# Performance work log

Measured on AMD Instinct MI355X. Metric: run time of the kernel, lower is better.

The kernel has to match this reference:

```python
import jax, jax.numpy as jnp
import numpy as np

NUM_NODES = 64
NUM_VISIBLE = 16
NUM_STEPS = 20
ENERGY_SCALE = 1.0


def setup_inputs() -> dict:
    key = jax.random.key(0)
    k1, k2, k3, k4 = jax.random.split(key, 4)
    B, E = 65536, 512
    embedding = jax.random.normal(k1, (B, E), dtype=jnp.float32)
    reward = jax.random.normal(k2, (B,), dtype=jnp.float32)
    pca_components = jax.random.normal(k3, (E, NUM_VISIBLE), dtype=jnp.float32)
    quadratic = jax.random.normal(k4, (NUM_NODES, NUM_NODES), dtype=jnp.float32) * 0.01
    return {"embedding": embedding, "reward": reward,
            "pca_components": pca_components, "quadratic": quadratic}


def reference(embedding, reward, pca_components, quadratic):
    B = embedding.shape[0]
    dtype = embedding.dtype

    # KPP fallback transform: PCA-style projection (B, E) @ (E, 16) -> (B, 16)
    rep = embedding @ pca_components
    visible_bias = rep[:, :NUM_VISIBLE]

    # per-sample linear bias, zeros except visible slots; BM bias = batch mean (no_grad)
    lb = jnp.zeros((B, NUM_NODES), dtype).at[:, :NUM_VISIBLE].set(visible_bias)
    b = jax.lax.stop_gradient(lb.mean(axis=0))  # (N,)

    # clamped visible state: sigmoid(2*r) broadcast to (B, NUM_VISIBLE)
    s_visible = jnp.broadcast_to(jax.nn.sigmoid(reward[:, None] * 2.0), (B, NUM_VISIBLE))

    Wsym = quadratic + quadratic.T  # symmetric coupling field

    key = jax.random.key(42)
    k_init, k_scan = jax.random.split(key)
    hidden0 = jax.random.bernoulli(k_init, 0.5, (B, NUM_NODES - NUM_VISIBLE)).astype(dtype)
    s0 = jnp.concatenate([s_visible, hidden0], axis=-1)  # (B, N)

    def gibbs_step(s, k):
        p = jax.nn.sigmoid(s @ Wsym + b)               # (B, N)
        s_new = jax.random.bernoulli(k, p).astype(dtype)
        s_new = s_new.at[:, :NUM_VISIBLE].set(s_visible)  # clamp visible units
        return s_new, None

    keys = jax.random.split(k_scan, NUM_STEPS)
    s_all, _ = jax.lax.scan(gibbs_step, s0, keys)

    # energy E(s) = -s^T Q s - b^T s  per sample
    energy = -jnp.einsum('bi,ij,bj->b', s_all, quadratic, s_all) - s_all @ b

    adjusted = reward - ENERGY_SCALE * energy
    return adjusted[:, None]  # (B, 1)
```

## Files before the change

### kernel.cpp

```cpp
#include <hip/hip_runtime.h>
#include <stdint.h>

#define NNODES 64
#define NVIS   16
#define NHID   48
#define NSTEPS 20
#define BATCH  65536
#define EDIM   512

typedef float f32x2 __attribute__((ext_vector_type(2)));
typedef float f32x4 __attribute__((ext_vector_type(4)));

__device__ __forceinline__ f32x2 pk_fma_lo(f32x2 s, f32x2 w, f32x2 c) {
  f32x2 d;
  asm("v_pk_fma_f32 %0, %1, %2, %3 op_sel:[0,0,0] op_sel_hi:[1,0,1]"
      : "=v"(d) : "v"(s), "v"(w), "v"(c));
  return d;
}
__device__ __forceinline__ f32x2 pk_fma_hi(f32x2 s, f32x2 w, f32x2 c) {
  f32x2 d;
  asm("v_pk_fma_f32 %0, %1, %2, %3 op_sel:[0,1,0] op_sel_hi:[1,1,1]"
      : "=v"(d) : "v"(s), "v"(w), "v"(c));
  return d;
}
__device__ __forceinline__ f32x2 pk_fma2(f32x2 a, f32x2 b, f32x2 c) {
  f32x2 d;
  asm("v_pk_fma_f32 %0, %1, %2, %3" : "=v"(d) : "v"(a), "v"(b), "v"(c));
  return d;
}
__device__ __forceinline__ f32x2 pk_mul2(f32x2 a, f32x2 b) {
  f32x2 d;
  asm("v_pk_mul_f32 %0, %1, %2" : "=v"(d) : "v"(a), "v"(b));
  return d;
}
__device__ __forceinline__ f32x2 pk_add2(f32x2 a, f32x2 b) {
  f32x2 d;
  asm("v_pk_add_f32 %0, %1, %2" : "=v"(d) : "v"(a), "v"(b));
  return d;
}
__device__ __forceinline__ f32x2 pk_sub2(f32x2 a, f32x2 b) {
  f32x2 d;
  asm("v_pk_add_f32 %0, %1, %2 neg_lo:[0,1] neg_hi:[0,1]" : "=v"(d) : "v"(a), "v"(b));
  return d;
}
__device__ __forceinline__ f32x2 pk_negsub2(f32x2 a, f32x2 b) {
  f32x2 d;
  asm("v_pk_add_f32 %0, %1, %2 neg_lo:[1,1] neg_hi:[1,1]" : "=v"(d) : "v"(a), "v"(b));
  return d;
}

__device__ __forceinline__ void tf2x32(uint32_t k0, uint32_t k1,
                                       uint32_t x0, uint32_t x1,
                                       uint32_t& o0, uint32_t& o1) {
  const uint32_t ks0 = k0, ks1 = k1, ks2 = k0 ^ k1 ^ 0x1BD11BDAu;
  x0 += ks0; x1 += ks1;
  const int rotA[4] = {13, 15, 26, 6};
  const int rotB[4] = {17, 29, 16, 24};
#pragma unroll
  for (int i = 0; i < 5; ++i) {
#pragma unroll
    for (int r = 0; r < 4; ++r) {
      const int rot = (i & 1) ? rotB[r] : rotA[r];
      x0 += x1;
      x1 = __builtin_rotateleft32(x1, rot);
      x1 ^= x0;
    }
    const uint32_t i0 = (i == 0 || i == 3) ? ks1 : (i == 1 || i == 4) ? ks2 : ks0;
    const uint32_t i1 = (i == 0 || i == 3) ? ks2 : (i == 1 || i == 4) ? ks0 : ks1;
    x0 += i0;
    x1 += i1 + (uint32_t)(i + 1);
  }
  o0 = x0; o1 = x1;
}

__device__ __forceinline__ uint32_t rbits32(uint32_t k0, uint32_t k1, uint32_t n) {
  uint32_t a, b;
  tf2x32(k0, k1, 0u, n, a, b);
  return a ^ b;
}

__device__ __forceinline__ f32x2 sigmoid2_pk(f32x2 a) {
#pragma clang fp contract(off)
  const f32x2 cL2En  = (f32x2)(-1.44269504088896341f);
  const f32x2 cHalf  = (f32x2)0.5f;
  const f32x2 cLn2Hi = (f32x2)0.693359375f;
  const f32x2 cLn2Lo = (f32x2)(-2.12194440e-4f);
  const f32x2 c0 = (f32x2)1.9875691500e-4f, c1 = (f32x2)1.3981999507e-3f;
  const f32x2 c2 = (f32x2)8.3334519073e-3f, c3 = (f32x2)4.1665795894e-2f;
  const f32x2 c4 = (f32x2)1.6666665459e-1f, c5 = (f32x2)5.0000001201e-1f;
  const f32x2 cOne = (f32x2)1.0f;

  f32x2 t = pk_fma2(a, cL2En, cHalf);
  f32x2 fx; fx.x = floorf(t.x); fx.y = floorf(t.y);
  f32x2 tmp = pk_mul2(fx, cLn2Hi);
  f32x2 z   = pk_mul2(fx, cLn2Lo);
  f32x2 xr  = pk_negsub2(a, tmp);
  xr = pk_sub2(xr, z);
  f32x2 zz = pk_mul2(xr, xr);
  f32x2 y = pk_fma2(xr, c0, c1);
  y = pk_fma2(y, xr, c2);
  y = pk_fma2(y, xr, c3);
  y = pk_fma2(y, xr, c4);
  y = pk_fma2(y, xr, c5);
  y = pk_fma2(y, zz, xr);
  y = pk_add2(y, cOne);
  int mx = (int)fx.x, my = (int)fx.y;
  f32x2 e;
  e.x = __int_as_float((mx + 127) << 23);
  e.y = __int_as_float((my + 127) << 23);
  f32x2 ex = pk_mul2(y, e);
  f32x2 den = pk_add2(ex, cOne);
  f32x2 r;
  r.x = 1.0f / den.x;
  r.y = 1.0f / den.y;
  return r;
}

__device__ __forceinline__ f32x2 dot_hidden(const f32x4* __restrict__ swq,
                                            const f32x2* wp, f32x2 acc16) {
  f32x2 acc = acc16;
#pragma unroll
  for (int i = 0; i < 24; ++i) {
    f32x4 q = swq[i];
    f32x2 slo; slo.x = q.x; slo.y = q.y;
    f32x2 shi; shi.x = q.z; shi.y = q.w;
    acc = pk_fma_lo(slo, wp[i], acc);
    acc = pk_fma_hi(shi, wp[i], acc);
  }
  return acc;
}

__global__ __launch_bounds__(512) void colsum_kernel(const float4* __restrict__ emb4,
                                                     float4* __restrict__ partials4,
                                                     int nblk) {
  __shared__ float4 red[4][128];
  const int t = threadIdx.x;
  const int c4 = t & 127, rs = t >> 7;
  float4 acc = make_float4(0.f, 0.f, 0.f, 0.f);
  const int stride = nblk * 4;
  for (int r = blockIdx.x * 4 + rs; r < BATCH; r += stride) {
    float4 v = emb4[(size_t)r * 128 + c4];
    acc.x += v.x; acc.y += v.y; acc.z += v.z; acc.w += v.w;
  }
  red[rs][c4] = acc;
  __syncthreads();
  if (rs == 0) {
    float4 a = red[0][c4], b = red[1][c4], c = red[2][c4], d = red[3][c4];
    float4 s;
    s.x = (a.x + b.x) + (c.x + d.x);
    s.y = (a.y + b.y) + (c.y + d.y);
    s.z = (a.z + b.z) + (c.z + d.z);
    s.w = (a.w + b.w) + (c.w + d.w);
    partials4[(size_t)blockIdx.x * 128 + c4] = s;
  }
}

__global__ __launch_bounds__(512) void reduce_kernel(const float* __restrict__ partials,
                                                     float* __restrict__ level2, int per) {
  const int t = threadIdx.x;
  float a = 0.0f;
  const int s0 = blockIdx.x * per;
  for (int s = s0; s < s0 + per; ++s) a += partials[(size_t)s * EDIM + t];
  level2[(size_t)blockIdx.x * EDIM + t] = a;
}

__global__ __launch_bounds__(512) void prep_kernel(const float* __restrict__ pca,
                                                   const float* __restrict__ level2, int g2,
                                                   float* __restrict__ bvec,
                                                   unsigned* __restrict__ keys) {
  __shared__ float cs[EDIM];
  int t = threadIdx.x;
  float a = 0.0f;
  for (int i = 0; i < g2; ++i) a += level2[(size_t)i * EDIM + t];
  cs[t] = a;
  __syncthreads();
  if (t < NNODES) {
    float bj = 0.0f;
    if (t < NVIS) {
      for (int e = 0; e < EDIM; ++e) bj = fmaf(cs[e], pca[e * NVIS + t], bj);
      bj *= (1.0f / 65536.0f);
    }
    bvec[t] = bj;
  }
  if (t == 0) {
    uint32_t ki0, ki1, ks0, ks1;
    tf2x32(0u, 42u, 0u, 0u, ki0, ki1);
    tf2x32(0u, 42u, 0u, 1u, ks0, ks1);
    keys[0] = ki0; keys[1] = ki1;
    for (int s = 0; s < NSTEPS; ++s) {
      uint32_t y0, y1;
      tf2x32(ks0, ks1, 0u, (uint32_t)s, y0, y1);
      keys[2 + 2 * s] = y0;
      keys[3 + 2 * s] = y1;
    }
  }
}

__global__ __launch_bounds__(256) void gibbs_kernel(const float* __restrict__ reward,
                                                    const float* __restrict__ quadratic,
                                                    const float* __restrict__ bvec,
                                                    const unsigned* __restrict__ keys,
                                                    float* __restrict__ out) {
#pragma clang fp contract(off)
  __shared__ float Wl[NNODES][NNODES];

  const int tid = threadIdx.x;
  for (int i = tid; i < NNODES * NNODES; i += 256) {
    int k = i >> 6, j = i & 63;
    Wl[k][j] = quadratic[i] + quadratic[j * NNODES + k];
  }
  __syncthreads();

  const int wave = tid >> 6, lane = tid & 63;

  const int r0 = (blockIdx.x * 4 + wave) * 2, r1 = r0 + 1;
  const float rw0 = reward[r0], rw1 = reward[r1];
  const float bj = bvec[lane];
  f32x2 sv2 = sigmoid2_pk((f32x2){-rw0 * 2.0f, -rw1 * 2.0f});
  sv2 = sigmoid2_pk((f32x2){rw0 * 2.0f, rw1 * 2.0f});

  f32x2 wp[24];
#pragma unroll
  for (int i = 0; i < 24; ++i) {
    f32x2 w; w.x = Wl[16 + 2 * i][lane]; w.y = Wl[17 + 2 * i][lane];
    wp[i] = w;
  }
  f32x2 acc16 = (f32x2)0.0f;
#pragma unroll
  for (int i = 0; i < 8; ++i) {
    f32x2 w; w.x = Wl[2 * i][lane]; w.y = Wl[2 * i + 1][lane];
    acc16 = pk_fma_lo(sv2, w, acc16);
    acc16 = pk_fma_hi(sv2, w, acc16);
  }
  __syncthreads();

  f32x2* sw = ((f32x2*)&Wl[0][0]) + wave * NHID;
  const f32x4* swq = (const f32x4*)sw;

  const bool isvis = (lane < NVIS);
  const uint32_t n0 = (uint32_t)(r0 * NNODES + lane);
  const uint32_t n1 = (uint32_t)(r1 * NNODES + lane);

  f32x2 scur = sv2;
  if (!isvis) {
    int jh = lane - NVIS;
    bool hb0 = (rbits32(keys[0], keys[1], (uint32_t)(r0 * NHID + jh)) >> 31) == 0u;
    bool hb1 = (rbits32(keys[0], keys[1], (uint32_t)(r1 * NHID + jh)) >> 31) == 0u;
    scur.x = hb0 ? 1.0f : 0.0f;
    scur.y = hb1 ? 1.0f : 0.0f;
    sw[jh] = scur;
  }

  const uint2* kbuf = (const uint2*)(keys + 2);
  const f32x2 cOneU = (f32x2)1.0f;
  uint2 kk = kbuf[0];
#pragma unroll 1
  for (int t = 0; t < NSTEPS; ++t) {
    uint2 kn = kbuf[(t + 1 < NSTEPS) ? t + 1 : t];
    uint32_t b0 = rbits32(kk.x, kk.y, n0);
    uint32_t b1 = rbits32(kk.x, kk.y, n1);
    f32x2 um;
    um.x = __uint_as_float((b0 >> 9) | 0x3f800000u);
    um.y = __uint_as_float((b1 >> 9) | 0x3f800000u);
    f32x2 u2 = pk_sub2(um, cOneU);
    f32x2 a2 = dot_hidden(swq, wp, acc16);
    f32x2 p2 = sigmoid2_pk(a2);
    if (!isvis) {
      scur.x = (u2.x < p2.x) ? 1.0f : 0.0f;
      scur.y = (u2.y < p2.y) ? 1.0f : 0.0f;
      sw[lane - NVIS] = scur;
    }
    kk = kn;
  }

  f32x2 a2 = dot_hidden(swq, wp, acc16);
  float c0 = scur.x * fmaf(0.5f, a2.x, bj);
  float c1 = scur.y * fmaf(0.5f, a2.y, bj);
#pragma unroll
  for (int off = 32; off; off >>= 1) {
    c0 += __shfl_xor(c0, off);
    c1 += __shfl_xor(c1, off);
  }
  if (lane == 0) {
    out[r0] = rw0 + c0;
    out[r1] = rw1 + c1;
  }
}

extern "C" void kernel_launch(void* const* d_in, const int* in_sizes, int n_in,
                              void* d_out, int out_size, void* d_ws, size_t ws_size,
                              hipStream_t stream) {
  const float* emb    = (const float*)d_in[0];
  const float* reward = (const float*)d_in[1];
  const float* pca    = (const float*)d_in[2];
  const float* quad   = (const float*)d_in[3];
  float* out = (float*)d_out;

  int nblk = 1024;
  while (nblk > 4 &&
         ws_size < (size_t)nblk * EDIM * 4 + (size_t)64 * EDIM * 4 + 4096)
    nblk >>= 1;
  const int g2  = (nblk >= 64) ? 64 : nblk;
  const int per = nblk / g2;

  float*    partials = (float*)d_ws;
  float*    level2   = partials + (size_t)nblk * EDIM;
  float*    bvec     = level2 + (size_t)64 * EDIM;
  unsigned* keys     = (unsigned*)(bvec + NNODES);

  colsum_kernel<<<nblk, 512, 0, stream>>>((const float4*)emb, (float4*)partials, nblk);
  reduce_kernel<<<g2, 512, 0, stream>>>(partials, level2, per);
  prep_kernel<<<1, 512, 0, stream>>>(pca, level2, g2, bvec, keys);
  gibbs_kernel<<<BATCH / 8, 256, 0, stream>>>(reward, quad, bvec, keys, out);
}
```

Before: 330.2 us.

## Process four rows per wave and generate RNG only for hidden units

Each wave now runs four batch rows instead of two, so the register-held coupling weights are reused across two packed accumulators and half as many blocks are launched. Random bits are drawn only for the 48 hidden units per row, three per lane, and passed through a per-wave LDS buffer. Before, every lane drew bits for all 64 nodes, including the 16 clamped visible ones. The trade-off is more LDS traffic, higher register pressure, and cross-lane LDS exchange inside a wave with no explicit barrier.

```diff
diff --git a/kernel.cpp b/kernel.cpp
--- a/kernel.cpp
+++ b/kernel.cpp
@@ -116,18 +116,24 @@
   return r;
 }
 
-__device__ __forceinline__ f32x2 dot_hidden(const f32x4* __restrict__ swq,
-                                            const f32x2* wp, f32x2 acc16) {
-  f32x2 acc = acc16;
+__device__ __forceinline__ void dot4(const f32x4* __restrict__ st,
+                                     const f32x2* wp, f32x2 a16A, f32x2 a16B,
+                                     f32x2& oA, f32x2& oB) {
+  f32x2 accA = a16A, accB = a16B;
 #pragma unroll
   for (int i = 0; i < 24; ++i) {
-    f32x4 q = swq[i];
-    f32x2 slo; slo.x = q.x; slo.y = q.y;
-    f32x2 shi; shi.x = q.z; shi.y = q.w;
-    acc = pk_fma_lo(slo, wp[i], acc);
-    acc = pk_fma_hi(shi, wp[i], acc);
-  }
-  return acc;
+    f32x4 q0 = st[2 * i];
+    f32x4 q1 = st[2 * i + 1];
+    f32x2 q0A; q0A.x = q0.x; q0A.y = q0.y;
+    f32x2 q0B; q0B.x = q0.z; q0B.y = q0.w;
+    f32x2 q1A; q1A.x = q1.x; q1A.y = q1.y;
+    f32x2 q1B; q1B.x = q1.z; q1B.y = q1.w;
+    accA = pk_fma_lo(q0A, wp[i], accA);
+    accA = pk_fma_hi(q1A, wp[i], accA);
+    accB = pk_fma_lo(q0B, wp[i], accB);
+    accB = pk_fma_hi(q1B, wp[i], accB);
+  }
+  oA = accA; oB = accB;
 }
 
 __global__ __launch_bounds__(512) void colsum_kernel(const float4* __restrict__ emb4,
@@ -203,6 +209,8 @@
                                                     float* __restrict__ out) {
 #pragma clang fp contract(off)
   __shared__ float Wl[NNODES][NNODES];
+  __shared__ float ubuf[4][4 * NHID];
+  __shared__ f32x4 sbuf[4][NHID];
 
   const int tid = threadIdx.x;
   for (int i = tid; i < NNODES * NNODES; i += 256) {
@@ -212,12 +220,13 @@
   __syncthreads();
 
   const int wave = tid >> 6, lane = tid & 63;
-
-  const int r0 = (blockIdx.x * 4 + wave) * 2, r1 = r0 + 1;
-  const float rw0 = reward[r0], rw1 = reward[r1];
+  const int gw = blockIdx.x * 4 + wave;
+  const int r0 = gw * 4;
+
+  const float4 rw4 = ((const float4*)reward)[gw];
   const float bj = bvec[lane];
-  f32x2 sv2 = sigmoid2_pk((f32x2){-rw0 * 2.0f, -rw1 * 2.0f});
-  sv2 = sigmoid2_pk((f32x2){rw0 * 2.0f, rw1 * 2.0f});
+  f32x2 svA = sigmoid2_pk((f32x2){rw4.x * 2.0f, rw4.y * 2.0f});
+  f32x2 svB = sigmoid2_pk((f32x2){rw4.z * 2.0f, rw4.w * 2.0f});
 
   f32x2 wp[24];
 #pragma unroll
@@ -225,65 +234,92 @@
     f32x2 w; w.x = Wl[16 + 2 * i][lane]; w.y = Wl[17 + 2 * i][lane];
     wp[i] = w;
   }
-  f32x2 acc16 = (f32x2)0.0f;
+  f32x2 acc16A = (f32x2)0.0f, acc16B = (f32x2)0.0f;
 #pragma unroll
   for (int i = 0; i < 8; ++i) {
     f32x2 w; w.x = Wl[2 * i][lane]; w.y = Wl[2 * i + 1][lane];
-    acc16 = pk_fma_lo(sv2, w, acc16);
-    acc16 = pk_fma_hi(sv2, w, acc16);
-  }
-  __syncthreads();
-
-  f32x2* sw = ((f32x2*)&Wl[0][0]) + wave * NHID;
-  const f32x4* swq = (const f32x4*)sw;
+    acc16A = pk_fma_lo(svA, w, acc16A);
+    acc16A = pk_fma_hi(svA, w, acc16A);
+    acc16B = pk_fma_lo(svB, w, acc16B);
+    acc16B = pk_fma_hi(svB, w, acc16B);
+  }
+
+  uint32_t nn[3];
+  float*   uw[3];
+  float*   s0p[3];
+  uint32_t ni[3];
+#pragma unroll
+  for (int c = 0; c < 3; ++c) {
+    int idx = c * 64 + lane;
+    int rr = (idx * 683) >> 15;
+    int jj = idx - rr * 48;
+    nn[c] = (uint32_t)((r0 + rr) * NNODES + NVIS + jj);
+    ni[c] = (uint32_t)((r0 + rr) * NHID + jj);
+    uw[c]  = &ubuf[wave][rr * NHID + jj];
+    s0p[c] = ((float*)&sbuf[wave][0]) + (jj * 4 + rr);
+  }
+
+  {
+    const uint32_t ki0 = keys[0], ki1 = keys[1];
+#pragma unroll
+    for (int c = 0; c < 3; ++c) {
+      uint32_t b = rbits32(ki0, ki1, ni[c]);
+      *s0p[c] = (b >> 31) ? 0.0f : 1.0f;
+    }
+  }
 
   const bool isvis = (lane < NVIS);
-  const uint32_t n0 = (uint32_t)(r0 * NNODES + lane);
-  const uint32_t n1 = (uint32_t)(r1 * NNODES + lane);
-
-  f32x2 scur = sv2;
-  if (!isvis) {
-    int jh = lane - NVIS;
-    bool hb0 = (rbits32(keys[0], keys[1], (uint32_t)(r0 * NHID + jh)) >> 31) == 0u;
-    bool hb1 = (rbits32(keys[0], keys[1], (uint32_t)(r1 * NHID + jh)) >> 31) == 0u;
-    scur.x = hb0 ? 1.0f : 0.0f;
-    scur.y = hb1 ? 1.0f : 0.0f;
-    sw[jh] = scur;
-  }
+  const int jc = isvis ? 0 : lane - NVIS;
+  f32x2 scurA = svA, scurB = svB;
+  const float* ub = ubuf[wave];
+  const f32x4* st = sbuf[wave];
 
   const uint2* kbuf = (const uint2*)(keys + 2);
-  const f32x2 cOneU = (f32x2)1.0f;
   uint2 kk = kbuf[0];
 #pragma unroll 1
   for (int t = 0; t < NSTEPS; ++t) {
     uint2 kn = kbuf[(t + 1 < NSTEPS) ? t + 1 : t];
-    uint32_t b0 = rbits32(kk.x, kk.y, n0);
-    uint32_t b1 = rbits32(kk.x, kk.y, n1);
-    f32x2 um;
-    um.x = __uint_as_float((b0 >> 9) | 0x3f800000u);
-    um.y = __uint_as_float((b1 >> 9) | 0x3f800000u);
-    f32x2 u2 = pk_sub2(um, cOneU);
-    f32x2 a2 = dot_hidden(swq, wp, acc16);
-    f32x2 p2 = sigmoid2_pk(a2);
+    uint32_t b0 = rbits32(kk.x, kk.y, nn[0]);
+    uint32_t b1 = rbits32(kk.x, kk.y, nn[1]);
+    uint32_t b2 = rbits32(kk.x, kk.y, nn[2]);
+    *uw[0] = __uint_as_float((b0 >> 9) | 0x3f800000u) - 1.0f;
+    *uw[1] = __uint_as_float((b1 >> 9) | 0x3f800000u) - 1.0f;
+    *uw[2] = __uint_as_float((b2 >> 9) | 0x3f800000u) - 1.0f;
+
+    f32x2 aA, aB;
+    dot4(st, wp, acc16A, acc16B, aA, aB);
+    f32x2 pA = sigmoid2_pk(aA);
+    f32x2 pB = sigmoid2_pk(aB);
+
+    f32x2 uA; uA.x = ub[jc];            uA.y = ub[NHID + jc];
+    f32x2 uB; uB.x = ub[2 * NHID + jc]; uB.y = ub[3 * NHID + jc];
     if (!isvis) {
-      scur.x = (u2.x < p2.x) ? 1.0f : 0.0f;
-      scur.y = (u2.y < p2.y) ? 1.0f : 0.0f;
-      sw[lane - NVIS] = scur;
+      scurA.x = (uA.x < pA.x) ? 1.0f : 0.0f;
+      scurA.y = (uA.y < pA.y) ? 1.0f : 0.0f;
+      scurB.x = (uB.x < pB.x) ? 1.0f : 0.0f;
+      scurB.y = (uB.y < pB.y) ? 1.0f : 0.0f;
+      f32x4 sq; sq.x = scurA.x; sq.y = scurA.y; sq.z = scurB.x; sq.w = scurB.y;
+      sbuf[wave][jc] = sq;
     }
     kk = kn;
   }
 
-  f32x2 a2 = dot_hidden(swq, wp, acc16);
-  float c0 = scur.x * fmaf(0.5f, a2.x, bj);
-  float c1 = scur.y * fmaf(0.5f, a2.y, bj);
+  f32x2 aA, aB;
+  dot4(st, wp, acc16A, acc16B, aA, aB);
+  f32x2 bj2; bj2.x = bj; bj2.y = bj;
+  const f32x2 half2 = (f32x2)0.5f;
+  f32x2 cA = pk_mul2(scurA, pk_fma2(half2, aA, bj2));
+  f32x2 cB = pk_mul2(scurB, pk_fma2(half2, aB, bj2));
+  float c0 = cA.x, c1 = cA.y, c2 = cB.x, c3 = cB.y;
 #pragma unroll
   for (int off = 32; off; off >>= 1) {
     c0 += __shfl_xor(c0, off);
     c1 += __shfl_xor(c1, off);
+    c2 += __shfl_xor(c2, off);
+    c3 += __shfl_xor(c3, off);
   }
   if (lane == 0) {
-    out[r0] = rw0 + c0;
-    out[r1] = rw1 + c1;
+    ((float4*)out)[gw] = make_float4(rw4.x + c0, rw4.y + c1, rw4.z + c2, rw4.w + c3);
   }
 }
 
@@ -311,5 +347,5 @@
   colsum_kernel<<<nblk, 512, 0, stream>>>((const float4*)emb, (float4*)partials, nblk);
   reduce_kernel<<<g2, 512, 0, stream>>>(partials, level2, per);
   prep_kernel<<<1, 512, 0, stream>>>(pca, level2, g2, bvec, keys);
-  gibbs_kernel<<<BATCH / 8, 256, 0, stream>>>(reward, quad, bvec, keys, out);
-}
+  gibbs_kernel<<<BATCH / 16, 256, 0, stream>>>(reward, quad, bvec, keys, out);
+}
```

Result: faster. 305.0 us (-7.6%).
